# Optimization experiments

Measured on AMD Instinct MI355X. Metric: run time of the kernel, lower is better.

## Reference

```python
import jax, jax.numpy as jnp
import numpy as np

N, E, D = 50000, 800000, 64  # nodes, edges, feature dim (all feature dims must match, see module)
EPS = 1e-5


def _linear_params(key, fin, fout):
    k1, k2 = jax.random.split(key)
    s = 1.0 / np.sqrt(fin)
    W = jax.random.uniform(k1, (fout, fin), minval=-s, maxval=s, dtype=jnp.float32)
    b = jax.random.uniform(k2, (fout,), minval=-s, maxval=s, dtype=jnp.float32)
    return W, b


def setup_inputs() -> dict:
    key = jax.random.key(0)
    ks = jax.random.split(key, 9)
    h = jax.random.normal(ks[0], (N, D), dtype=jnp.float32)
    e = jax.random.normal(ks[1], (E, D), dtype=jnp.float32)
    src = jax.random.randint(ks[2], (E,), 0, N)
    dst = jax.random.randint(ks[3], (E,), 0, N)
    W_upd, b_upd = _linear_params(ks[4], 3 * D, D)   # upd_linear: cat(h_src,h_dst,e) -> D
    W_act, b_act = _linear_params(ks[5], D, D)       # activation_linear
    W_gd, b_gd = _linear_params(ks[6], D, D)         # gating_dst_linear
    W_gs, b_gs = _linear_params(ks[7], D, D)         # gating_src_linear
    W_out, b_out = _linear_params(ks[8], D, D)       # final linear
    g_un = jnp.ones((D,), jnp.float32); be_un = jnp.zeros((D,), jnp.float32)  # upd_norm gamma/beta
    g_gn = jnp.ones((D,), jnp.float32); be_gn = jnp.zeros((D,), jnp.float32)  # gating_norm gamma/beta
    return dict(h=h, e=e, src=src, dst=dst,
                W_upd=W_upd, b_upd=b_upd, g_un=g_un, be_un=be_un,
                W_act=W_act, b_act=b_act, W_gd=W_gd, b_gd=b_gd,
                W_gs=W_gs, b_gs=b_gs, g_gn=g_gn, be_gn=be_gn,
                W_out=W_out, b_out=b_out)


def _batchnorm(x, gamma, beta):
    # nn.BatchNorm1d in training mode: biased batch stats over axis 0
    m = x.mean(axis=0)
    v = x.var(axis=0)
    return (x - m) * jax.lax.rsqrt(v + EPS) * gamma + beta


def reference(h, e, src, dst, W_upd, b_upd, g_un, be_un, W_act, b_act,
              W_gd, b_gd, W_gs, b_gs, g_gn, be_gn, W_out, b_out):
    n_nodes = h.shape[0]
    # --- edge update: gather endpoints, linear, batchnorm, SiLU, residual ---
    e_cat = jnp.concatenate([h[src], h[dst], e], axis=1)       # [E, 3D]
    e_lin = e_cat @ W_upd.T + b_upd                             # [E, D]
    e2 = e + jax.nn.silu(_batchnorm(e_lin, g_un, be_un))        # residual (dims equal)
    # --- edge softmax grouped by destination node ---
    logit = e2 @ W_act.T + b_act                                # [E, D]
    mx = jax.ops.segment_max(logit, dst, num_segments=n_nodes)  # [N, D]
    ex = jnp.exp(logit - mx[dst])
    den = jax.ops.segment_sum(ex, dst, num_segments=n_nodes)
    a = ex / den[dst]                                           # [E, D]
    # --- gated aggregation: mail = a * W_gd h_dst, scatter-sum to dst ---
    mail = a * (h[dst] @ W_gd.T + b_gd)                         # [E, D]
    agg = jax.ops.segment_sum(mail, dst, num_segments=n_nodes)  # [N, D]
    h2 = (h @ W_gs.T + b_gs) + agg
    h2 = jax.nn.silu(_batchnorm(h2, g_gn, be_gn)) + h
    h2 = h2 @ W_out.T + b_out
    return (h2, e2)
```

## Files before the change

kernel.cpp:

```cpp
#include <hip/hip_runtime.h>

#define N_NODES 50000
#define N_EDGES 800000
#define EPS_BN 1e-5f


typedef __attribute__((ext_vector_type(8))) short s16x8;
typedef __attribute__((ext_vector_type(4))) float f32x4;

__device__ __forceinline__ unsigned short f2bf(float f) {
  unsigned int u = __float_as_uint(f);
  u += 0x7FFFu + ((u >> 16) & 1u);
  return (unsigned short)(u >> 16);
}
__device__ __forceinline__ unsigned int pack2(float lo, float hi) {
  return (unsigned int)f2bf(lo) | ((unsigned int)f2bf(hi) << 16);
}
__device__ __forceinline__ s16x8 cvt8(float4 a, float4 b) {
  union { s16x8 v; unsigned int u[4]; } r;
  r.u[0] = pack2(a.x, a.y); r.u[1] = pack2(a.z, a.w);
  r.u[2] = pack2(b.x, b.y); r.u[3] = pack2(b.z, b.w);
  return r.v;
}
__device__ __forceinline__ float siluf(float x) { return x / (1.f + __expf(-x)); }

__global__ void k_pre(unsigned int* __restrict__ wsu,
                      const float* __restrict__ W_upd, const float* __restrict__ W_gd,
                      const float* __restrict__ W_gs, const float* __restrict__ W_out,
                      const float* __restrict__ h, short* __restrict__ hbf) {
  int b = blockIdx.x;
  if (b < 49) {
    int i = b * 256 + threadIdx.x;
    if (i < 512) wsu[i] = 0u;
    if (i < 12500) wsu[12800 + i] = 0u;
    if (i < 6144) {
      int s = i >> 2, w = i & 3;
      int row = s / 24, slot = s - row * 24;
      int ii = slot ^ (row & 7);
      int fidx = row * 192 + ii * 8 + w * 2;
      wsu[512 + i] = pack2(W_upd[fidx], W_upd[fidx + 1]);
    }
    if (i < 2048) {
      float2 a = *(const float2*)&W_gd[(size_t)i * 2];
      float2 bb = *(const float2*)&W_gs[(size_t)i * 2];
      float2 c = *(const float2*)&W_out[(size_t)i * 2];
      wsu[6656 + i] = pack2(a.x, a.y);
      wsu[8704 + i] = pack2(bb.x, bb.y);
      wsu[10752 + i] = pack2(c.x, c.y);
    }
  } else {
    int t = (b - 49) * 256 + threadIdx.x;
    if (t < (N_NODES * 64) / 8) {
      float4 a = *(const float4*)&h[(size_t)t * 8];
      float4 bb = *(const float4*)&h[(size_t)t * 8 + 4];
      *(s16x8*)&hbf[(size_t)t * 8] = cvt8(a, bb);
    }
  }
}

__global__ void k_flags(const int* __restrict__ dst, unsigned char* __restrict__ flb) {
  int i = blockIdx.x * 256 + threadIdx.x;
  if (i < N_EDGES) flb[dst[i]] = 1;
}

template<int PHASE>
__global__ __launch_bounds__(256, 4) void k_edge(
    const short* __restrict__ hbf, const float* __restrict__ e,
    const int* __restrict__ src, const int* __restrict__ dst,
    const unsigned int* __restrict__ wsu, const float* __restrict__ b_upd,
    const float* __restrict__ ws, float* __restrict__ out_e)
{
  __shared__ short Bls[64 * 192];
  __shared__ float red[4][128];

  int tid = threadIdx.x;
  int ln = tid & 63, wv = tid >> 6;
  int lr = ln & 15, lq = ln >> 4, lk = lq * 8;
  int m0 = blockIdx.x * 128;
  int r0 = wv * 32 + lr, r1 = r0 + 16;
  int mA = m0 + r0, mB = m0 + r1;

  const float* pe0 = e + (size_t)mA * 64 + lk;
  const float* pe1 = e + (size_t)mB * 64 + lk;
  float4 e0a = *(const float4*)(pe0);
  float4 e0b = *(const float4*)(pe0 + 4);
  float4 e0c = *(const float4*)(pe0 + 32);
  float4 e0d = *(const float4*)(pe0 + 36);
  float4 e1a = *(const float4*)(pe1);
  float4 e1b = *(const float4*)(pe1 + 4);
  float4 e1c = *(const float4*)(pe1 + 32);
  float4 e1d = *(const float4*)(pe1 + 36);

  int s0 = src[mA], d0 = dst[mA];
  int s1i = src[mB], d1 = dst[mB];

  s16x8 A0[6], A1[6];
  A0[0] = *(const s16x8*)&hbf[s0 * 64 + lk];
  A0[1] = *(const s16x8*)&hbf[s0 * 64 + 32 + lk];
  A0[2] = *(const s16x8*)&hbf[d0 * 64 + lk];
  A0[3] = *(const s16x8*)&hbf[d0 * 64 + 32 + lk];
  A1[0] = *(const s16x8*)&hbf[s1i * 64 + lk];
  A1[1] = *(const s16x8*)&hbf[s1i * 64 + 32 + lk];
  A1[2] = *(const s16x8*)&hbf[d1 * 64 + lk];
  A1[3] = *(const s16x8*)&hbf[d1 * 64 + 32 + lk];

  {
    unsigned int* bls32 = (unsigned int*)Bls;
    #pragma unroll
    for (int j = 0; j < 6; ++j) {
      int base = (j * 4 + wv) * 256;
      __builtin_amdgcn_global_load_lds(
          (__attribute__((address_space(1))) void*)(unsigned int*)(wsu + 512 + base + ln * 4),
          (__attribute__((address_space(3))) void*)(bls32 + base),
          16, 0, 0);
    }
  }

  A0[4] = cvt8(e0a, e0b);
  A0[5] = cvt8(e0c, e0d);
  A1[4] = cvt8(e1a, e1b);
  A1[5] = cvt8(e1c, e1d);
  __syncthreads();

  int rl = ln >> 4, c0 = (ln & 15) * 4;
  float4 epre[2][4];
  if (PHASE == 1) {
    #pragma unroll
    for (int rt = 0; rt < 2; ++rt)
      #pragma unroll
      for (int q = 0; q < 4; ++q)
        epre[rt][q] = *(const float4*)&e[(size_t)(m0 + wv * 32 + rt * 16 + rl * 4 + q) * 64 + c0];
  }

  f32x4 zero4 = {0.f, 0.f, 0.f, 0.f};
  f32x4 acc[2][4];
  #pragma unroll
  for (int rt = 0; rt < 2; ++rt)
    #pragma unroll
    for (int ct = 0; ct < 4; ++ct) acc[rt][ct] = zero4;

  #pragma unroll
  for (int ct = 0; ct < 4; ++ct) {
    int row = ct * 16 + lr, r7 = row & 7;
    #pragma unroll
    for (int kk = 0; kk < 6; ++kk) {
      s16x8 b = *(const s16x8*)&Bls[row * 192 + (((kk * 4 + lq) ^ r7) << 3)];
      acc[0][ct] = __builtin_amdgcn_mfma_f32_16x16x32_bf16(A0[kk], b, acc[0][ct], 0, 0, 0);
      acc[1][ct] = __builtin_amdgcn_mfma_f32_16x16x32_bf16(A1[kk], b, acc[1][ct], 0, 0, 0);
    }
  }

  if (PHASE == 0) {
    float s1[4], s2[4];
    #pragma unroll
    for (int ct = 0; ct < 4; ++ct) {
      float bias = b_upd[ct * 16 + lr];
      float a1s = 0.f, a2s = 0.f;
      #pragma unroll
      for (int rt = 0; rt < 2; ++rt)
        #pragma unroll
        for (int q = 0; q < 4; ++q) {
          float v = acc[rt][ct][q] + bias;
          a1s += v; a2s += v * v;
        }
      s1[ct] = a1s; s2[ct] = a2s;
    }
    #pragma unroll
    for (int ct = 0; ct < 4; ++ct) {
      s1[ct] += __shfl_xor(s1[ct], 16); s1[ct] += __shfl_xor(s1[ct], 32);
      s2[ct] += __shfl_xor(s2[ct], 16); s2[ct] += __shfl_xor(s2[ct], 32);
    }
    if (ln < 16) {
      #pragma unroll
      for (int ct = 0; ct < 4; ++ct) {
        red[wv][ct * 16 + ln] = s1[ct];
        red[wv][64 + ct * 16 + ln] = s2[ct];
      }
    }
    __syncthreads();
    if (tid < 128) {
      float t = red[0][tid] + red[1][tid] + red[2][tid] + red[3][tid];
      out_e[(size_t)blockIdx.x * 128 + tid] = t;
    }
  } else {
    #pragma unroll
    for (int ct = 0; ct < 4; ++ct) {
      int col = ct * 16 + lr;
      float scale = ws[128 + col], shift = ws[192 + col], bias = b_upd[col];
      #pragma unroll
      for (int rt = 0; rt < 2; ++rt)
        #pragma unroll
        for (int q = 0; q < 4; ++q) {
          float x = acc[rt][ct][q] + bias;
          acc[rt][ct][q] = siluf(x * scale + shift);
        }
    }
    __syncthreads();
    float* T = (float*)((char*)Bls + wv * 1280);
    #pragma unroll
    for (int rt = 0; rt < 2; ++rt) {
      #pragma unroll
      for (int q = 0; q < 4; ++q) {
        #pragma unroll
        for (int ct = 0; ct < 4; ++ct)
          T[lq * 72 + ct * 16 + lr] = acc[rt][ct][q];
        float4 t4 = *(const float4*)&T[rl * 72 + c0];
        float4 ev = epre[rt][q];
        t4.x += ev.x; t4.y += ev.y; t4.z += ev.z; t4.w += ev.w;
        *(float4*)&out_e[(size_t)(m0 + wv * 32 + rt * 16 + rl * 4 + q) * 64 + c0] = t4;
      }
    }
  }
}

__global__ void k_red(const float* __restrict__ partials, float* __restrict__ ws) {
  __shared__ float sred[256];
  int c = blockIdx.x;
  float s = 0.f;
  for (int i = threadIdx.x; i < N_EDGES / 128; i += 256)
    s += partials[(size_t)i * 128 + c];
  sred[threadIdx.x] = s;
  __syncthreads();
  for (int off = 128; off >= 1; off >>= 1) {
    if (threadIdx.x < off) sred[threadIdx.x] += sred[threadIdx.x + off];
    __syncthreads();
  }
  if (threadIdx.x == 0) ws[c] = sred[0];
}

__global__ void k_fin(float* __restrict__ ws, const float* __restrict__ gamma,
                      const float* __restrict__ beta, float rcount, int off) {
  int d = threadIdx.x;
  float mean = ws[off + d] * rcount;
  float var = ws[off + 64 + d] * rcount - mean * mean;
  float inv = rsqrtf(var + EPS_BN);
  float a = inv * gamma[d];
  ws[off + 128 + d] = a;
  ws[off + 192 + d] = beta[d] - mean * a;
}

__global__ __launch_bounds__(256, 4) void k_nstat(
    const short* __restrict__ hbf, const unsigned int* __restrict__ wsu,
    const unsigned char* __restrict__ flb,
    const float* __restrict__ b_gd, const float* __restrict__ b_gs,
    float* __restrict__ ws)
{
  __shared__ short Bgd[64 * 64], Bgs[64 * 64];
  __shared__ float red[4][128];
  int tid = threadIdx.x;
  int ln = tid & 63, wv = tid >> 6;
  int lr = ln & 15, lq = ln >> 4, lk = lq * 8;
  int n0 = blockIdx.x * 128;

  const uint4* Sgd = (const uint4*)(wsu + 6656);
  const uint4* Sgs = (const uint4*)(wsu + 8704);
  #pragma unroll
  for (int j = 0; j < 2; ++j) {
    int c = tid + j * 256;
    int row = c >> 3, i = c & 7, sl = row * 8 + (i ^ (row & 7));
    ((uint4*)Bgd)[sl] = Sgd[c];
    ((uint4*)Bgs)[sl] = Sgs[c];
  }

  int r0 = wv * 32 + lr, r1 = r0 + 16;
  int nA = min(n0 + r0, N_NODES - 1), nB = min(n0 + r1, N_NODES - 1);
  s16x8 A0[2], A1[2];
  A0[0] = *(const s16x8*)&hbf[nA * 64 + lk];
  A0[1] = *(const s16x8*)&hbf[nA * 64 + 32 + lk];
  A1[0] = *(const s16x8*)&hbf[nB * 64 + lk];
  A1[1] = *(const s16x8*)&hbf[nB * 64 + 32 + lk];
  __syncthreads();

  f32x4 zero4 = {0.f, 0.f, 0.f, 0.f};
  f32x4 accd[2][4], accs[2][4];
  #pragma unroll
  for (int rt = 0; rt < 2; ++rt)
    #pragma unroll
    for (int ct = 0; ct < 4; ++ct) { accd[rt][ct] = zero4; accs[rt][ct] = zero4; }

  #pragma unroll
  for (int ct = 0; ct < 4; ++ct) {
    int row = ct * 16 + lr, r7 = row & 7;
    #pragma unroll
    for (int kk = 0; kk < 2; ++kk) {
      int sl = ((kk * 4 + lq) ^ r7) << 3;
      s16x8 bd = *(const s16x8*)&Bgd[row * 64 + sl];
      s16x8 bs = *(const s16x8*)&Bgs[row * 64 + sl];
      accd[0][ct] = __builtin_amdgcn_mfma_f32_16x16x32_bf16(A0[kk], bd, accd[0][ct], 0, 0, 0);
      accd[1][ct] = __builtin_amdgcn_mfma_f32_16x16x32_bf16(A1[kk], bd, accd[1][ct], 0, 0, 0);
      accs[0][ct] = __builtin_amdgcn_mfma_f32_16x16x32_bf16(A0[kk], bs, accs[0][ct], 0, 0, 0);
      accs[1][ct] = __builtin_amdgcn_mfma_f32_16x16x32_bf16(A1[kk], bs, accs[1][ct], 0, 0, 0);
    }
  }

  float s1[4], s2[4];
  #pragma unroll
  for (int ct = 0; ct < 4; ++ct) {
    int col = ct * 16 + lr;
    float bd = b_gd[col], bs = b_gs[col];
    float a1s = 0.f, a2s = 0.f;
    #pragma unroll
    for (int rt = 0; rt < 2; ++rt)
      #pragma unroll
      for (int q = 0; q < 4; ++q) {
        int row = wv * 32 + rt * 16 + lq * 4 + q;
        int n = n0 + row;
        if (n < N_NODES) {
          float fl = (float)flb[n];
          float v = accs[rt][ct][q] + bs + fl * (accd[rt][ct][q] + bd);
          a1s += v; a2s += v * v;
        }
      }
    s1[ct] = a1s; s2[ct] = a2s;
  }
  #pragma unroll
  for (int ct = 0; ct < 4; ++ct) {
    s1[ct] += __shfl_xor(s1[ct], 16); s1[ct] += __shfl_xor(s1[ct], 32);
    s2[ct] += __shfl_xor(s2[ct], 16); s2[ct] += __shfl_xor(s2[ct], 32);
  }
  if (ln < 16) {
    #pragma unroll
    for (int ct = 0; ct < 4; ++ct) {
      red[wv][ct * 16 + ln] = s1[ct];
      red[wv][64 + ct * 16 + ln] = s2[ct];
    }
  }
  __syncthreads();
  if (tid < 128) {
    float t = red[0][tid] + red[1][tid] + red[2][tid] + red[3][tid];
    atomicAdd(&ws[256 + tid], t);
  }
}

__global__ __launch_bounds__(256, 4) void k_nout(
    const float* __restrict__ h, const short* __restrict__ hbf,
    const unsigned int* __restrict__ wsu,
    const unsigned char* __restrict__ flb,
    const float* __restrict__ b_gd, const float* __restrict__ b_gs,
    const float* __restrict__ b_out, const float* __restrict__ ws,
    float* __restrict__ out_h)
{
  __shared__ short R1[128 * 64];
  __shared__ short R2[64 * 64];
  int tid = threadIdx.x;
  int ln = tid & 63, wv = tid >> 6;
  int lr = ln & 15, lq = ln >> 4, lk = lq * 8;
  int n0 = blockIdx.x * 128;

  const uint4* Sgd = (const uint4*)(wsu + 6656);
  const uint4* Sgs = (const uint4*)(wsu + 8704);
  const uint4* Sot = (const uint4*)(wsu + 10752);
  short* Bgd = R1;
  short* Bgs = R1 + 4096;
  #pragma unroll
  for (int j = 0; j < 2; ++j) {
    int c = tid + j * 256;
    int row = c >> 3, i = c & 7, sl = row * 8 + (i ^ (row & 7));
    ((uint4*)Bgd)[sl] = Sgd[c];
    ((uint4*)Bgs)[sl] = Sgs[c];
    ((uint4*)R2)[sl] = Sot[c];
  }

  int r0 = wv * 32 + lr, r1 = r0 + 16;
  int nA = min(n0 + r0, N_NODES - 1), nB = min(n0 + r1, N_NODES - 1);
  s16x8 A0[2], A1[2];
  A0[0] = *(const s16x8*)&hbf[nA * 64 + lk];
  A0[1] = *(const s16x8*)&hbf[nA * 64 + 32 + lk];
  A1[0] = *(const s16x8*)&hbf[nB * 64 + lk];
  A1[1] = *(const s16x8*)&hbf[nB * 64 + 32 + lk];
  __syncthreads();

  f32x4 zero4 = {0.f, 0.f, 0.f, 0.f};
  f32x4 accd[2][4], accs[2][4];
  #pragma unroll
  for (int rt = 0; rt < 2; ++rt)
    #pragma unroll
    for (int ct = 0; ct < 4; ++ct) { accd[rt][ct] = zero4; accs[rt][ct] = zero4; }

  #pragma unroll
  for (int ct = 0; ct < 4; ++ct) {
    int row = ct * 16 + lr, r7 = row & 7;
    #pragma unroll
    for (int kk = 0; kk < 2; ++kk) {
      int sl = ((kk * 4 + lq) ^ r7) << 3;
      s16x8 bd = *(const s16x8*)&Bgd[row * 64 + sl];
      s16x8 bs = *(const s16x8*)&Bgs[row * 64 + sl];
      accd[0][ct] = __builtin_amdgcn_mfma_f32_16x16x32_bf16(A0[kk], bd, accd[0][ct], 0, 0, 0);
      accd[1][ct] = __builtin_amdgcn_mfma_f32_16x16x32_bf16(A1[kk], bd, accd[1][ct], 0, 0, 0);
      accs[0][ct] = __builtin_amdgcn_mfma_f32_16x16x32_bf16(A0[kk], bs, accs[0][ct], 0, 0, 0);
      accs[1][ct] = __builtin_amdgcn_mfma_f32_16x16x32_bf16(A1[kk], bs, accs[1][ct], 0, 0, 0);
    }
  }

  float tv[4][2][4];
  #pragma unroll
  for (int ct = 0; ct < 4; ++ct) {
    int col = ct * 16 + lr;
    float a_n = ws[384 + col], b_n = ws[448 + col];
    float bd = b_gd[col], bs = b_gs[col];
    #pragma unroll
    for (int rt = 0; rt < 2; ++rt)
      #pragma unroll
      for (int q = 0; q < 4; ++q) {
        int row = wv * 32 + rt * 16 + lq * 4 + q;
        int n = min(n0 + row, N_NODES - 1);
        float fl = (float)flb[n];
        float v = accs[rt][ct][q] + bs + fl * (accd[rt][ct][q] + bd);
        tv[ct][rt][q] = siluf(v * a_n + b_n) + h[(size_t)n * 64 + col];
      }
  }
  __syncthreads();
  #pragma unroll
  for (int ct = 0; ct < 4; ++ct) {
    int col = ct * 16 + lr;
    #pragma unroll
    for (int rt = 0; rt < 2; ++rt)
      #pragma unroll
      for (int q = 0; q < 4; ++q) {
        int row = wv * 32 + rt * 16 + lq * 4 + q;
        R1[row * 64 + (((col >> 3) ^ (row & 7)) << 3) + (col & 7)] = (short)f2bf(tv[ct][rt][q]);
      }
  }
  __syncthreads();

  s16x8 T0[2], T1[2];
  #pragma unroll
  for (int kk = 0; kk < 2; ++kk) {
    T0[kk] = *(const s16x8*)&R1[r0 * 64 + (((kk * 4 + lq) ^ (r0 & 7)) << 3)];
    T1[kk] = *(const s16x8*)&R1[r1 * 64 + (((kk * 4 + lq) ^ (r1 & 7)) << 3)];
  }
  f32x4 ac2[2][4];
  #pragma unroll
  for (int rt = 0; rt < 2; ++rt)
    #pragma unroll
    for (int ct = 0; ct < 4; ++ct) ac2[rt][ct] = zero4;
  #pragma unroll
  for (int ct = 0; ct < 4; ++ct) {
    int row = ct * 16 + lr, r7 = row & 7;
    #pragma unroll
    for (int kk = 0; kk < 2; ++kk) {
      s16x8 b = *(const s16x8*)&R2[row * 64 + (((kk * 4 + lq) ^ r7) << 3)];
      ac2[0][ct] = __builtin_amdgcn_mfma_f32_16x16x32_bf16(T0[kk], b, ac2[0][ct], 0, 0, 0);
      ac2[1][ct] = __builtin_amdgcn_mfma_f32_16x16x32_bf16(T1[kk], b, ac2[1][ct], 0, 0, 0);
    }
  }
  #pragma unroll
  for (int ct = 0; ct < 4; ++ct) {
    int col = ct * 16 + lr;
    float bo = b_out[col];
    #pragma unroll
    for (int rt = 0; rt < 2; ++rt)
      #pragma unroll
      for (int q = 0; q < 4; ++q) {
        int row = wv * 32 + rt * 16 + lq * 4 + q;
        int n = n0 + row;
        if (n < N_NODES) out_h[(size_t)n * 64 + col] = ac2[rt][ct][q] + bo;
      }
  }
}

extern "C" void kernel_launch(void* const* d_in, const int* in_sizes, int n_in,
                              void* d_out, int out_size, void* d_ws, size_t ws_size,
                              hipStream_t stream) {
  const float* h     = (const float*)d_in[0];
  const float* e     = (const float*)d_in[1];
  const int*   src   = (const int*)d_in[2];
  const int*   dst   = (const int*)d_in[3];
  const float* W_upd = (const float*)d_in[4];
  const float* b_upd = (const float*)d_in[5];
  const float* g_un  = (const float*)d_in[6];
  const float* be_un = (const float*)d_in[7];
  const float* W_gd  = (const float*)d_in[10];
  const float* b_gd  = (const float*)d_in[11];
  const float* W_gs  = (const float*)d_in[12];
  const float* b_gs  = (const float*)d_in[13];
  const float* g_gn  = (const float*)d_in[14];
  const float* be_gn = (const float*)d_in[15];
  const float* W_out = (const float*)d_in[16];
  const float* b_out = (const float*)d_in[17];

  float* outH = (float*)d_out;
  float* outE = outH + (size_t)N_NODES * 64;
  float* ws = (float*)d_ws;
  unsigned int* wsu = (unsigned int*)d_ws;
  unsigned char* flb = (unsigned char*)(wsu + 12800);
  short* hbf = (short*)(wsu + 25600);

  k_pre<<<49 + 1563, 256, 0, stream>>>(wsu, W_upd, W_gd, W_gs, W_out, h, hbf);
  k_flags<<<(N_EDGES + 255) / 256, 256, 0, stream>>>(dst, flb);
  k_edge<0><<<N_EDGES / 128, 256, 0, stream>>>(hbf, e, src, dst, wsu, b_upd, ws, outH);
  k_red<<<128, 256, 0, stream>>>(outH, ws);
  k_fin<<<1, 64, 0, stream>>>(ws, g_un, be_un, 1.f / (float)N_EDGES, 0);
  k_edge<1><<<N_EDGES / 128, 256, 0, stream>>>(hbf, e, src, dst, wsu, b_upd, ws, outE);
  k_nstat<<<(N_NODES + 127) / 128, 256, 0, stream>>>(hbf, wsu, flb, b_gd, b_gs, ws);
  k_fin<<<1, 64, 0, stream>>>(ws, g_gn, be_gn, 1.f / (float)N_NODES, 256);
  k_nout<<<(N_NODES + 127) / 128, 256, 0, stream>>>(h, hbf, wsu, flb, b_gd, b_gs, b_out, ws, outH);
}
```

Before: 240.9 us.

## Fuse flag kernel into edge pass, merge BN reduce+finalize, stash node pre-activations

Sets the destination-node flags inside the first edge pass instead of in a separate k_flags kernel. It merges the edge batch-norm reduction and finalize into one kernel, which computes both moments per block. k_nstat now writes its pre-norm node values into the output buffer, so k_nout reads them back instead of recomputing the gating matmuls. It also raises the occupancy hint for phase 0. This removes launches and duplicated MFMA work, at the cost of an extra 12.8MB write and read of node activations. k_nout reads and overwrites the same buffer in place, and each block touches only its own rows.

```diff
diff --git a/kernel.cpp b/kernel.cpp
--- a/kernel.cpp
+++ b/kernel.cpp
@@ -58,17 +58,13 @@
   }
 }
 
-__global__ void k_flags(const int* __restrict__ dst, unsigned char* __restrict__ flb) {
-  int i = blockIdx.x * 256 + threadIdx.x;
-  if (i < N_EDGES) flb[dst[i]] = 1;
-}
-
 template<int PHASE>
-__global__ __launch_bounds__(256, 4) void k_edge(
+__global__ __launch_bounds__(256, PHASE == 0 ? 5 : 4) void k_edge(
     const short* __restrict__ hbf, const float* __restrict__ e,
     const int* __restrict__ src, const int* __restrict__ dst,
     const unsigned int* __restrict__ wsu, const float* __restrict__ b_upd,
-    const float* __restrict__ ws, float* __restrict__ out_e)
+    const float* __restrict__ ws, unsigned char* __restrict__ flb,
+    float* __restrict__ out_e)
 {
   __shared__ short Bls[64 * 192];
   __shared__ float red[4][128];
@@ -94,6 +90,8 @@
   int s0 = src[mA], d0 = dst[mA];
   int s1i = src[mB], d1 = dst[mB];
 
+  if (PHASE == 0 && lq == 0) { flb[d0] = 1; flb[d1] = 1; }
+
   s16x8 A0[6], A1[6];
   A0[0] = *(const s16x8*)&hbf[s0 * 64 + lk];
   A0[1] = *(const s16x8*)&hbf[s0 * 64 + 32 + lk];
@@ -213,19 +211,32 @@
   }
 }
 
-__global__ void k_red(const float* __restrict__ partials, float* __restrict__ ws) {
-  __shared__ float sred[256];
+__global__ void k_redfin(const float* __restrict__ partials, float* __restrict__ ws,
+                         const float* __restrict__ gamma, const float* __restrict__ beta,
+                         float rcount) {
+  __shared__ float sr[2][256];
   int c = blockIdx.x;
-  float s = 0.f;
-  for (int i = threadIdx.x; i < N_EDGES / 128; i += 256)
-    s += partials[(size_t)i * 128 + c];
-  sred[threadIdx.x] = s;
+  float s1 = 0.f, s2 = 0.f;
+  for (int i = threadIdx.x; i < N_EDGES / 128; i += 256) {
+    s1 += partials[(size_t)i * 128 + c];
+    s2 += partials[(size_t)i * 128 + 64 + c];
+  }
+  sr[0][threadIdx.x] = s1; sr[1][threadIdx.x] = s2;
   __syncthreads();
   for (int off = 128; off >= 1; off >>= 1) {
-    if (threadIdx.x < off) sred[threadIdx.x] += sred[threadIdx.x + off];
+    if (threadIdx.x < off) {
+      sr[0][threadIdx.x] += sr[0][threadIdx.x + off];
+      sr[1][threadIdx.x] += sr[1][threadIdx.x + off];
+    }
     __syncthreads();
   }
-  if (threadIdx.x == 0) ws[c] = sred[0];
+  if (threadIdx.x == 0) {
+    float mean = sr[0][0] * rcount;
+    float var = sr[1][0] * rcount - mean * mean;
+    float a = rsqrtf(var + EPS_BN) * gamma[c];
+    ws[128 + c] = a;
+    ws[192 + c] = beta[c] - mean * a;
+  }
 }
 
 __global__ void k_fin(float* __restrict__ ws, const float* __restrict__ gamma,
@@ -243,7 +254,7 @@
     const short* __restrict__ hbf, const unsigned int* __restrict__ wsu,
     const unsigned char* __restrict__ flb,
     const float* __restrict__ b_gd, const float* __restrict__ b_gs,
-    float* __restrict__ ws)
+    float* __restrict__ ws, float* __restrict__ v_out)
 {
   __shared__ short Bgd[64 * 64], Bgs[64 * 64];
   __shared__ float red[4][128];
@@ -308,6 +319,7 @@
         if (n < N_NODES) {
           float fl = (float)flb[n];
           float v = accs[rt][ct][q] + bs + fl * (accd[rt][ct][q] + bd);
+          v_out[(size_t)n * 64 + col] = v;
           a1s += v; a2s += v * v;
         }
       }
@@ -333,102 +345,54 @@
 }
 
 __global__ __launch_bounds__(256, 4) void k_nout(
-    const float* __restrict__ h, const short* __restrict__ hbf,
-    const unsigned int* __restrict__ wsu,
-    const unsigned char* __restrict__ flb,
-    const float* __restrict__ b_gd, const float* __restrict__ b_gs,
+    const float* __restrict__ h, const unsigned int* __restrict__ wsu,
     const float* __restrict__ b_out, const float* __restrict__ ws,
-    float* __restrict__ out_h)
+    const float* __restrict__ v_in, float* __restrict__ out_h)
 {
   __shared__ short R1[128 * 64];
   __shared__ short R2[64 * 64];
   int tid = threadIdx.x;
   int ln = tid & 63, wv = tid >> 6;
-  int lr = ln & 15, lq = ln >> 4, lk = lq * 8;
+  int lr = ln & 15, lq = ln >> 4;
   int n0 = blockIdx.x * 128;
 
-  const uint4* Sgd = (const uint4*)(wsu + 6656);
-  const uint4* Sgs = (const uint4*)(wsu + 8704);
   const uint4* Sot = (const uint4*)(wsu + 10752);
-  short* Bgd = R1;
-  short* Bgs = R1 + 4096;
   #pragma unroll
   for (int j = 0; j < 2; ++j) {
     int c = tid + j * 256;
     int row = c >> 3, i = c & 7, sl = row * 8 + (i ^ (row & 7));
-    ((uint4*)Bgd)[sl] = Sgd[c];
-    ((uint4*)Bgs)[sl] = Sgs[c];
     ((uint4*)R2)[sl] = Sot[c];
   }
 
+  int c0 = (tid & 15) * 4;
+  int rbase = tid >> 4;
+  float4 scl = *(const float4*)&ws[384 + c0];
+  float4 shf = *(const float4*)&ws[448 + c0];
+  #pragma unroll
+  for (int i = 0; i < 8; ++i) {
+    int row = rbase + 16 * i;
+    int n = min(n0 + row, N_NODES - 1);
+    float4 v4 = *(const float4*)&v_in[(size_t)n * 64 + c0];
+    float4 h4 = *(const float4*)&h[(size_t)n * 64 + c0];
+    float tx = siluf(v4.x * scl.x + shf.x) + h4.x;
+    float ty = siluf(v4.y * scl.y + shf.y) + h4.y;
+    float tz = siluf(v4.z * scl.z + shf.z) + h4.z;
+    float tw = siluf(v4.w * scl.w + shf.w) + h4.w;
+    int sl = ((((c0 >> 3) ^ (row & 7)) << 3) | (c0 & 7));
+    unsigned int* p = (unsigned int*)&R1[row * 64 + sl];
+    p[0] = pack2(tx, ty);
+    p[1] = pack2(tz, tw);
+  }
+  __syncthreads();
+
   int r0 = wv * 32 + lr, r1 = r0 + 16;
-  int nA = min(n0 + r0, N_NODES - 1), nB = min(n0 + r1, N_NODES - 1);
-  s16x8 A0[2], A1[2];
-  A0[0] = *(const s16x8*)&hbf[nA * 64 + lk];
-  A0[1] = *(const s16x8*)&hbf[nA * 64 + 32 + lk];
-  A1[0] = *(const s16x8*)&hbf[nB * 64 + lk];
-  A1[1] = *(const s16x8*)&hbf[nB * 64 + 32 + lk];
-  __syncthreads();
-
-  f32x4 zero4 = {0.f, 0.f, 0.f, 0.f};
-  f32x4 accd[2][4], accs[2][4];
-  #pragma unroll
-  for (int rt = 0; rt < 2; ++rt)
-    #pragma unroll
-    for (int ct = 0; ct < 4; ++ct) { accd[rt][ct] = zero4; accs[rt][ct] = zero4; }
-
-  #pragma unroll
-  for (int ct = 0; ct < 4; ++ct) {
-    int row = ct * 16 + lr, r7 = row & 7;
-    #pragma unroll
-    for (int kk = 0; kk < 2; ++kk) {
-      int sl = ((kk * 4 + lq) ^ r7) << 3;
-      s16x8 bd = *(const s16x8*)&Bgd[row * 64 + sl];
-      s16x8 bs = *(const s16x8*)&Bgs[row * 64 + sl];
-      accd[0][ct] = __builtin_amdgcn_mfma_f32_16x16x32_bf16(A0[kk], bd, accd[0][ct], 0, 0, 0);
-      accd[1][ct] = __builtin_amdgcn_mfma_f32_16x16x32_bf16(A1[kk], bd, accd[1][ct], 0, 0, 0);
-      accs[0][ct] = __builtin_amdgcn_mfma_f32_16x16x32_bf16(A0[kk], bs, accs[0][ct], 0, 0, 0);
-      accs[1][ct] = __builtin_amdgcn_mfma_f32_16x16x32_bf16(A1[kk], bs, accs[1][ct], 0, 0, 0);
-    }
-  }
-
-  float tv[4][2][4];
-  #pragma unroll
-  for (int ct = 0; ct < 4; ++ct) {
-    int col = ct * 16 + lr;
-    float a_n = ws[384 + col], b_n = ws[448 + col];
-    float bd = b_gd[col], bs = b_gs[col];
-    #pragma unroll
-    for (int rt = 0; rt < 2; ++rt)
-      #pragma unroll
-      for (int q = 0; q < 4; ++q) {
-        int row = wv * 32 + rt * 16 + lq * 4 + q;
-        int n = min(n0 + row, N_NODES - 1);
-        float fl = (float)flb[n];
-        float v = accs[rt][ct][q] + bs + fl * (accd[rt][ct][q] + bd);
-        tv[ct][rt][q] = siluf(v * a_n + b_n) + h[(size_t)n * 64 + col];
-      }
-  }
-  __syncthreads();
-  #pragma unroll
-  for (int ct = 0; ct < 4; ++ct) {
-    int col = ct * 16 + lr;
-    #pragma unroll
-    for (int rt = 0; rt < 2; ++rt)
-      #pragma unroll
-      for (int q = 0; q < 4; ++q) {
-        int row = wv * 32 + rt * 16 + lq * 4 + q;
-        R1[row * 64 + (((col >> 3) ^ (row & 7)) << 3) + (col & 7)] = (short)f2bf(tv[ct][rt][q]);
-      }
-  }
-  __syncthreads();
-
   s16x8 T0[2], T1[2];
   #pragma unroll
   for (int kk = 0; kk < 2; ++kk) {
     T0[kk] = *(const s16x8*)&R1[r0 * 64 + (((kk * 4 + lq) ^ (r0 & 7)) << 3)];
     T1[kk] = *(const s16x8*)&R1[r1 * 64 + (((kk * 4 + lq) ^ (r1 & 7)) << 3)];
   }
+  f32x4 zero4 = {0.f, 0.f, 0.f, 0.f};
   f32x4 ac2[2][4];
   #pragma unroll
   for (int rt = 0; rt < 2; ++rt)
@@ -487,12 +451,10 @@
   short* hbf = (short*)(wsu + 25600);
 
   k_pre<<<49 + 1563, 256, 0, stream>>>(wsu, W_upd, W_gd, W_gs, W_out, h, hbf);
-  k_flags<<<(N_EDGES + 255) / 256, 256, 0, stream>>>(dst, flb);
-  k_edge<0><<<N_EDGES / 128, 256, 0, stream>>>(hbf, e, src, dst, wsu, b_upd, ws, outH);
-  k_red<<<128, 256, 0, stream>>>(outH, ws);
-  k_fin<<<1, 64, 0, stream>>>(ws, g_un, be_un, 1.f / (float)N_EDGES, 0);
-  k_edge<1><<<N_EDGES / 128, 256, 0, stream>>>(hbf, e, src, dst, wsu, b_upd, ws, outE);
-  k_nstat<<<(N_NODES + 127) / 128, 256, 0, stream>>>(hbf, wsu, flb, b_gd, b_gs, ws);
+  k_edge<0><<<N_EDGES / 128, 256, 0, stream>>>(hbf, e, src, dst, wsu, b_upd, ws, flb, outH);
+  k_redfin<<<64, 256, 0, stream>>>(outH, ws, g_un, be_un, 1.f / (float)N_EDGES);
+  k_edge<1><<<N_EDGES / 128, 256, 0, stream>>>(hbf, e, src, dst, wsu, b_upd, ws, flb, outE);
+  k_nstat<<<(N_NODES + 127) / 128, 256, 0, stream>>>(hbf, wsu, flb, b_gd, b_gs, ws, outH);
   k_fin<<<1, 64, 0, stream>>>(ws, g_gn, be_gn, 1.f / (float)N_NODES, 256);
-  k_nout<<<(N_NODES + 127) / 128, 256, 0, stream>>>(h, hbf, wsu, flb, b_gd, b_gs, b_out, ws, outH);
-}
+  k_nout<<<(N_NODES + 127) / 128, 256, 0, stream>>>(h, wsu, b_out, ws, outH, outH);
+}
```

After: 241.7 us. No clear change (+0.4%).
